# Kernel optimization log

Measured on AMD Instinct MI355X. Metric: run time of the kernel, lower is better.

The kernel has to match this reference:

```python
import jax, jax.numpy as jnp
import numpy as np

N_NODES = 50000
N_EDGES = 800000
IN_CH = 128
HID = 64
OUT_CH = 64


def sage_conv(x, src, dst, w_l, w_r, b, num_nodes):
    """PyG SAGEConv with mean aggregation: lin_l(mean_j x_j) + lin_r(x_i)."""
    # gather source features and scatter-mean into destination nodes
    agg = jax.ops.segment_sum(x[src], dst, num_segments=num_nodes)          # [N, C]
    deg = jax.ops.segment_sum(jnp.ones((src.shape[0],), x.dtype), dst,
                              num_segments=num_nodes)                        # [N]
    mean = agg / jnp.maximum(deg, 1.0)[:, None]
    return mean @ w_l + x @ w_r + b


def setup_inputs() -> dict:
    key = jax.random.key(0)
    k = jax.random.split(key, 8)
    x = jax.random.normal(k[0], (N_NODES, IN_CH), dtype=jnp.float32)
    edge_index = jax.random.randint(k[1], (2, N_EDGES), 0, N_NODES, dtype=jnp.int32)
    s1 = 1.0 / np.sqrt(IN_CH)
    s2 = 1.0 / np.sqrt(HID)
    w1_l = jax.random.uniform(k[2], (IN_CH, HID), jnp.float32, -s1, s1)
    w1_r = jax.random.uniform(k[3], (IN_CH, HID), jnp.float32, -s1, s1)
    b1 = jax.random.uniform(k[4], (HID,), jnp.float32, -s1, s1)
    w2_l = jax.random.uniform(k[5], (HID, OUT_CH), jnp.float32, -s2, s2)
    w2_r = jax.random.uniform(k[6], (HID, OUT_CH), jnp.float32, -s2, s2)
    b2 = jax.random.uniform(k[7], (OUT_CH,), jnp.float32, -s2, s2)
    return {"x": x, "edge_index": edge_index,
            "w1_l": w1_l, "w1_r": w1_r, "b1": b1,
            "w2_l": w2_l, "w2_r": w2_r, "b2": b2}


def reference(x, edge_index, w1_l, w1_r, b1, w2_l, w2_r, b2):
    src, dst = edge_index[0], edge_index[1]
    num_nodes = x.shape[0]
    h = jax.nn.relu(sage_conv(x, src, dst, w1_l, w1_r, b1, num_nodes))
    out = jax.nn.relu(sage_conv(h, src, dst, w2_l, w2_r, b2, num_nodes))
    return out
```

## Files before the change

### kernel.cpp

```cpp
#include <hip/hip_runtime.h>
#include <hip/hip_fp16.h>

#define DEGCAP 64
#define NB_MAX 256
#define BCAP 5120
#define TILE 4000

typedef _Float16 half8 __attribute__((ext_vector_type(8)));
typedef float float4v __attribute__((ext_vector_type(4)));

__global__ __launch_bounds__(256) void prep(int* __restrict__ bCursor,
                                            const float* __restrict__ w1l,
                                            const float* __restrict__ w1r,
                                            const float* __restrict__ w2l,
                                            const float* __restrict__ w2r,
                                            _Float16* __restrict__ Wt1,
                                            _Float16* __restrict__ Wt2) {
    const int gtid = blockIdx.x * 256 + threadIdx.x;
    const int gstride = gridDim.x * 256;
    if (gtid < NB_MAX) bCursor[gtid] = 0;
    for (int i = gtid; i < 128 * 128; i += gstride) {
        int c = i >> 7, k = i & 127;
        const float* W = (c < 64) ? w1l : w1r;
        Wt1[c * 128 + k] = (_Float16)W[k * 64 + (c & 63)];
    }
    for (int i = gtid; i < 128 * 64; i += gstride) {
        int c = i >> 6, k = i & 63;
        const float* W = (c < 64) ? w2l : w2r;
        Wt2[c * 64 + k] = (_Float16)W[k * 64 + (c & 63)];
    }
}

template <int K>
__device__ __forceinline__ void gemm_body_f32(const float* __restrict__ Av,
                                              const _Float16* __restrict__ Wt,
                                              unsigned short* __restrict__ Clh,
                                              unsigned short* __restrict__ Trh,
                                              int M, int blk) {
    constexpr int NS = K / 32;
    const int tid = threadIdx.x;
    const int row0 = blk * 64;
    const int wv = tid >> 6;
    const int lane = tid & 63;
    const int qd = lane >> 4;
    const int lr = lane & 15;
    const int col = wv * 16 + lr;

    half8 bl[NS], br[NS];
    #pragma unroll
    for (int s = 0; s < NS; ++s) {
        bl[s] = *(const half8*)&Wt[col * K + s * 32 + qd * 8];
        br[s] = *(const half8*)&Wt[(64 + col) * K + s * 32 + qd * 8];
    }

    half8 a[4][NS];
    #pragma unroll
    for (int i = 0; i < 4; ++i) {
        const int gr = row0 + i * 16 + lr;
        const bool ok = gr < M;
        const float* Arow = Av + (long long)gr * K;
        #pragma unroll
        for (int s = 0; s < NS; ++s) {
            float4 t0 = make_float4(0.f, 0.f, 0.f, 0.f);
            float4 t1 = make_float4(0.f, 0.f, 0.f, 0.f);
            if (ok) {
                t0 = *(const float4*)&Arow[s * 32 + qd * 8];
                t1 = *(const float4*)&Arow[s * 32 + qd * 8 + 4];
            }
            half8 h;
            h[0] = (_Float16)t0.x; h[1] = (_Float16)t0.y;
            h[2] = (_Float16)t0.z; h[3] = (_Float16)t0.w;
            h[4] = (_Float16)t1.x; h[5] = (_Float16)t1.y;
            h[6] = (_Float16)t1.z; h[7] = (_Float16)t1.w;
            a[i][s] = h;
        }
    }

    float4v accL[4], accR[4];
    #pragma unroll
    for (int i = 0; i < 4; ++i) {
        accL[i] = (float4v){0.f, 0.f, 0.f, 0.f};
        accR[i] = (float4v){0.f, 0.f, 0.f, 0.f};
    }

    #pragma unroll
    for (int i = 0; i < 4; ++i) {
        #pragma unroll
        for (int s = 0; s < NS; ++s) {
            accL[i] = __builtin_amdgcn_mfma_f32_16x16x32_f16(a[i][s], bl[s], accL[i], 0, 0, 0);
            accR[i] = __builtin_amdgcn_mfma_f32_16x16x32_f16(a[i][s], br[s], accR[i], 0, 0, 0);
        }
    }

    #pragma unroll
    for (int i = 0; i < 4; ++i) {
        #pragma unroll
        for (int rg = 0; rg < 4; ++rg) {
            int gr = row0 + i * 16 + qd * 4 + rg;
            if (gr < M) {
                Clh[(long long)gr * 64 + col] = __half_as_ushort(__float2half_rn(accL[i][rg]));
                Trh[(long long)gr * 64 + col] = __half_as_ushort(__float2half_rn(accR[i][rg]));
            }
        }
    }
}

__global__ __launch_bounds__(256) void fused_scatter_gemm1(
        const int* __restrict__ src, const int* __restrict__ dst,
        int* __restrict__ bCursor, unsigned int* __restrict__ gPacked,
        int E, int NB, int scatterBlocks,
        const float* __restrict__ A, const _Float16* __restrict__ Wt1,
        unsigned short* __restrict__ Clh, unsigned short* __restrict__ Trh,
        int M) {
    __shared__ __align__(16) char smem[22048];
    const int tid = threadIdx.x;

    if ((int)blockIdx.x < scatterBlocks) {
        unsigned int* spv = (unsigned int*)smem;
        unsigned char* sbuk = (unsigned char*)(smem + 16000);
        int* hist = (int*)(smem + 20000);
        int* cur  = (int*)(smem + 21024);

        const int t0 = blockIdx.x * TILE;
        const int len = (E - t0) < TILE ? (E - t0) : TILE;

        hist[tid] = 0;
        __syncthreads();
        for (int j = tid; j < len; j += 256) {
            int d = dst[t0 + j];
            int s = src[t0 + j];
            int b = d >> 8;
            sbuk[j] = (unsigned char)b;
            spv[j] = ((unsigned int)(d & 255) << 17) | (unsigned int)s;
            atomicAdd(&hist[b], 1);
        }
        __syncthreads();
        if (tid < NB && hist[tid] > 0)
            cur[tid] = tid * BCAP + atomicAdd(&bCursor[tid], hist[tid]);
        __syncthreads();
        for (int j = tid; j < len; j += 256) {
            int b = sbuk[j];
            int pos = atomicAdd(&cur[b], 1);
            if (pos < (b + 1) * BCAP) gPacked[pos] = spv[j];
        }
    } else {
        gemm_body_f32<128>(A, Wt1, Clh, Trh, M, (int)blockIdx.x - scatterBlocks);
    }
}

__global__ __launch_bounds__(256) void bucket_build(const unsigned int* __restrict__ gPacked,
                                                    const int* __restrict__ bCursor,
                                                    int* __restrict__ deg,
                                                    unsigned short* __restrict__ ssrc,
                                                    int N) {
    __shared__ int cnt[256];
    const int tid = threadIdx.x;
    const int b = blockIdx.x;
    const int base = b * BCAP;
    int C = bCursor[b];
    if (C > BCAP) C = BCAP;

    cnt[tid] = 0;
    __syncthreads();
    for (int j = tid; j < C; j += 256) {
        unsigned int v = gPacked[base + j];
        int ln = v >> 17;
        int pos = atomicAdd(&cnt[ln], 1);
        if (pos < DEGCAP)
            ssrc[(long long)(b * 256 + ln) * DEGCAP + pos] = (unsigned short)(v & 0x1FFFFu);
    }
    __syncthreads();
    int node = b * 256 + tid;
    if (node < N) deg[node] = cnt[tid] < DEGCAP ? cnt[tid] : DEGCAP;
}

__device__ __forceinline__ float4 agg_node(const uint2* __restrict__ TL,
                                           const uint2* __restrict__ TR,
                                           const float* __restrict__ bias,
                                           const int* __restrict__ deg_,
                                           const uint2* __restrict__ ssrc2,
                                           int w, int lane, int c, bool ok) {
    const int deg = ok ? deg_[w] : 0;
    const int n = deg < DEGCAP ? deg : DEGCAP;
    uint2 su = ok ? ssrc2[(size_t)w * 16 + c] : make_uint2(0u, 0u);

    float a0 = 0.f, a1 = 0.f, a2 = 0.f, a3 = 0.f;
    for (int j = 0; j < n; j += 4) {
        const int b = (lane & 48) + (j >> 2);
        unsigned sx = __shfl((int)su.x, b, 64);
        unsigned sy = __shfl((int)su.y, b, 64);
        int e0 = (int)(sx & 0xFFFFu);
        int e1 = (int)(sx >> 16);
        int e2 = (int)(sy & 0xFFFFu);
        int e3 = (int)(sy >> 16);
        uint2 q0 = TL[e0 * 16 + c];
        uint2 q1 = TL[e1 * 16 + c];
        uint2 q2 = TL[e2 * 16 + c];
        uint2 q3 = TL[e3 * 16 + c];
        float2 f;
        f = __half22float2(*(__half2*)&q0.x); a0 += f.x; a1 += f.y;
        f = __half22float2(*(__half2*)&q0.y); a2 += f.x; a3 += f.y;
        if (j + 1 < n) {
            f = __half22float2(*(__half2*)&q1.x); a0 += f.x; a1 += f.y;
            f = __half22float2(*(__half2*)&q1.y); a2 += f.x; a3 += f.y;
        }
        if (j + 2 < n) {
            f = __half22float2(*(__half2*)&q2.x); a0 += f.x; a1 += f.y;
            f = __half22float2(*(__half2*)&q2.y); a2 += f.x; a3 += f.y;
        }
        if (j + 3 < n) {
            f = __half22float2(*(__half2*)&q3.x); a0 += f.x; a1 += f.y;
            f = __half22float2(*(__half2*)&q3.y); a2 += f.x; a3 += f.y;
        }
    }

    float4 r = make_float4(0.f, 0.f, 0.f, 0.f);
    if (ok) {
        float d = (float)(deg > 1 ? deg : 1);
        uint2 tu = TR[(size_t)w * 16 + c];
        float2 t0 = __half22float2(*(__half2*)&tu.x);
        float2 t1 = __half22float2(*(__half2*)&tu.y);
        float4 bb = *(const float4*)&bias[c * 4];
        r.x = fmaxf(a0 / d + t0.x + bb.x, 0.f);
        r.y = fmaxf(a1 / d + t0.y + bb.y, 0.f);
        r.z = fmaxf(a2 / d + t1.x + bb.z, 0.f);
        r.w = fmaxf(a3 / d + t1.y + bb.w, 0.f);
    }
    return r;
}

__global__ __launch_bounds__(256) void agg1_gemm2(const uint2* __restrict__ TL,
                                                  const uint2* __restrict__ TR,
                                                  const float* __restrict__ b1,
                                                  const int* __restrict__ deg_,
                                                  const uint2* __restrict__ ssrc2,
                                                  const _Float16* __restrict__ Wt2,
                                                  unsigned short* __restrict__ Cl2,
                                                  unsigned short* __restrict__ Tr2,
                                                  int N) {
    __shared__ _Float16 xs[16 * 72];
    const int tid = threadIdx.x;
    const int wv = tid >> 6;
    const int lane = tid & 63;
    const int c = lane & 15;
    const int row = wv * 4 + (lane >> 4);
    const int w = (int)blockIdx.x * 16 + row;
    const bool ok = w < N;

    float4 h = agg_node(TL, TR, b1, deg_, ssrc2, w, lane, c, ok);
    {
        __half2 h0 = __floats2half2_rn(h.x, h.y);
        __half2 h1 = __floats2half2_rn(h.z, h.w);
        uint2 st;
        st.x = *(unsigned int*)&h0;
        st.y = *(unsigned int*)&h1;
        *(uint2*)&xs[row * 72 + c * 4] = st;
    }
    __syncthreads();

    const int qd = lane >> 4;
    const int lr = lane & 15;
    const int col = wv * 16 + lr;
    const int row0 = (int)blockIdx.x * 16;

    half8 bl[2], br[2], a[2];
    #pragma unroll
    for (int s = 0; s < 2; ++s) {
        bl[s] = *(const half8*)&Wt2[col * 64 + s * 32 + qd * 8];
        br[s] = *(const half8*)&Wt2[(64 + col) * 64 + s * 32 + qd * 8];
        a[s]  = *(const half8*)&xs[lr * 72 + s * 32 + qd * 8];
    }

    float4v accL = (float4v){0.f, 0.f, 0.f, 0.f};
    float4v accR = (float4v){0.f, 0.f, 0.f, 0.f};
    #pragma unroll
    for (int s = 0; s < 2; ++s) {
        accL = __builtin_amdgcn_mfma_f32_16x16x32_f16(a[s], bl[s], accL, 0, 0, 0);
        accR = __builtin_amdgcn_mfma_f32_16x16x32_f16(a[s], br[s], accR, 0, 0, 0);
    }

    #pragma unroll
    for (int rg = 0; rg < 4; ++rg) {
        int gr = row0 + qd * 4 + rg;
        if (gr < N) {
            Cl2[(long long)gr * 64 + col] = __half_as_ushort(__float2half_rn(accL[rg]));
            Tr2[(long long)gr * 64 + col] = __half_as_ushort(__float2half_rn(accR[rg]));
        }
    }
}

__global__ __launch_bounds__(256) void agg2(const uint2* __restrict__ TL,
                                            const uint2* __restrict__ TR,
                                            const float* __restrict__ bias,
                                            const int* __restrict__ deg_,
                                            const uint2* __restrict__ ssrc2,
                                            float* __restrict__ outv, int N) {
    const int tid = threadIdx.x;
    const int wv = tid >> 6;
    const int lane = tid & 63;
    const int c = lane & 15;
    const int w = (int)blockIdx.x * 16 + wv * 4 + (lane >> 4);
    const bool ok = w < N;

    float4 r = agg_node(TL, TR, bias, deg_, ssrc2, w, lane, c, ok);
    if (ok)
        ((float4*)outv)[(size_t)w * 16 + c] = r;
}

extern "C" void kernel_launch(void* const* d_in, const int* in_sizes, int n_in,
                              void* d_out, int out_size, void* d_ws, size_t ws_size,
                              hipStream_t stream) {
    const float* x   = (const float*)d_in[0];
    const int*   ei  = (const int*)d_in[1];
    const float* w1l = (const float*)d_in[2];
    const float* w1r = (const float*)d_in[3];
    const float* b1  = (const float*)d_in[4];
    const float* w2l = (const float*)d_in[5];
    const float* w2r = (const float*)d_in[6];
    const float* b2  = (const float*)d_in[7];
    float* out = (float*)d_out;

    const int N = in_sizes[0] / 128;
    const int E = in_sizes[1] / 2;
    const int* src = ei;
    const int* dst = ei + E;
    const int NB = (N + 255) >> 8;

    auto alignup = [](size_t v) { return (v + 255) & ~(size_t)255; };
    char* p = (char*)d_ws;
    int* bCursor = (int*)p;                    p += alignup(NB_MAX * sizeof(int));
    int* deg     = (int*)p;                    p += alignup((size_t)N * sizeof(int));
    unsigned int* gPacked = (unsigned int*)p;  p += alignup((size_t)NB_MAX * BCAP * sizeof(unsigned int));
    unsigned short* ssrc = (unsigned short*)p; p += alignup((size_t)N * DEGCAP * sizeof(unsigned short));
    const long long NC = (long long)N * 64;
    unsigned short* tlh = (unsigned short*)p;  p += alignup((size_t)NC * sizeof(unsigned short));
    unsigned short* tl2 = (unsigned short*)p;  p += alignup((size_t)NC * sizeof(unsigned short));
    unsigned short* trh = (unsigned short*)p;  p += alignup((size_t)NC * sizeof(unsigned short));
    unsigned short* tr2 = (unsigned short*)p;  p += alignup((size_t)NC * sizeof(unsigned short));
    _Float16* Wt1 = (_Float16*)p;              p += alignup(128 * 128 * sizeof(_Float16));
    _Float16* Wt2 = (_Float16*)p;              p += alignup(128 * 64 * sizeof(_Float16));

    const int scatterBlocks = (E + TILE - 1) / TILE;
    const int gemmBlocks = (N + 63) / 64;
    const int aggBlocks = (N + 15) / 16;

    prep<<<96, 256, 0, stream>>>(bCursor, w1l, w1r, w2l, w2r, Wt1, Wt2);

    fused_scatter_gemm1<<<scatterBlocks + gemmBlocks, 256, 0, stream>>>(
        src, dst, bCursor, gPacked, E, NB, scatterBlocks,
        x, Wt1, tlh, trh, N);

    bucket_build<<<NB, 256, 0, stream>>>(gPacked, bCursor, deg, ssrc, N);

    agg1_gemm2<<<aggBlocks, 256, 0, stream>>>((const uint2*)tlh,
                                              (const uint2*)trh,
                                              b1, deg, (const uint2*)ssrc,
                                              Wt2, tl2, tr2, N);

    agg2<<<aggBlocks, 256, 0, stream>>>((const uint2*)tl2,
                                        (const uint2*)tr2,
                                        b2, deg, (const uint2*)ssrc,
                                        out, N);
}
```

Before: 163.6 us.

## Fuse bucket build into layer-1 aggregation and second GEMM kernel

Merges the bucket_build kernel with agg1_gemm2: each block takes a 32-node slice of a 256-node bucket, builds that slice's neighbour lists in shared memory, writes them and the degrees out for agg2, then aggregates and runs the second-layer MFMA on 32 rows. This removes one kernel launch and the global round trip of the neighbour lists before layer 1. In exchange, each of the eight sub-blocks rescans the whole bucket's packed edge list and keeps only one eighth, so bucket reads rise eightfold. Grid parallelism also changes from N/16 blocks to NB*8 blocks of 32 nodes.

```diff
diff --git a/kernel.cpp b/kernel.cpp
--- a/kernel.cpp
+++ b/kernel.cpp
@@ -5,6 +5,7 @@
 #define NB_MAX 256
 #define BCAP 5120
 #define TILE 4000
+#define SUBB 8
 
 typedef _Float16 half8 __attribute__((ext_vector_type(8)));
 typedef float float4v __attribute__((ext_vector_type(4)));
@@ -148,30 +149,156 @@
     }
 }
 
-__global__ __launch_bounds__(256) void bucket_build(const unsigned int* __restrict__ gPacked,
-                                                    const int* __restrict__ bCursor,
-                                                    int* __restrict__ deg,
-                                                    unsigned short* __restrict__ ssrc,
-                                                    int N) {
-    __shared__ int cnt[256];
+__global__ __launch_bounds__(256) void bb_agg1_gemm2(
+        const unsigned int* __restrict__ gPacked,
+        const int* __restrict__ bCursor,
+        const uint2* __restrict__ TL, const uint2* __restrict__ TR,
+        const float* __restrict__ bias,
+        const _Float16* __restrict__ Wt2,
+        unsigned short* __restrict__ ssrc_out,
+        int* __restrict__ deg_out,
+        unsigned short* __restrict__ Cl2,
+        unsigned short* __restrict__ Tr2,
+        int N) {
+    __shared__ unsigned short ssrcT[32 * 64];
+    __shared__ int cnt[32];
+    __shared__ int degL[32];
+    __shared__ _Float16 xs[32 * 72];
     const int tid = threadIdx.x;
-    const int b = blockIdx.x;
-    const int base = b * BCAP;
-    int C = bCursor[b];
+    const int B = (int)blockIdx.x >> 3;
+    const int oct = (int)blockIdx.x & 7;
+    const int node0 = B * 256 + oct * 32;
+
+    if (tid < 32) cnt[tid] = 0;
+    __syncthreads();
+    int C = bCursor[B];
     if (C > BCAP) C = BCAP;
-
-    cnt[tid] = 0;
+    const unsigned int* gp = gPacked + B * BCAP;
+    for (int j = tid; j < C; j += 256) {
+        unsigned int v = gp[j];
+        int ln = v >> 17;
+        if ((ln >> 5) == oct) {
+            int l = ln & 31;
+            int pos = atomicAdd(&cnt[l], 1);
+            if (pos < DEGCAP)
+                ssrcT[l * 64 + pos] = (unsigned short)(v & 0x1FFFFu);
+        }
+    }
     __syncthreads();
-    for (int j = tid; j < C; j += 256) {
-        unsigned int v = gPacked[base + j];
-        int ln = v >> 17;
-        int pos = atomicAdd(&cnt[ln], 1);
-        if (pos < DEGCAP)
-            ssrc[(long long)(b * 256 + ln) * DEGCAP + pos] = (unsigned short)(v & 0x1FFFFu);
+    if (tid < 32) {
+        int d = cnt[tid] < DEGCAP ? cnt[tid] : DEGCAP;
+        degL[tid] = d;
+        int node = node0 + tid;
+        if (node < N) deg_out[node] = d;
     }
     __syncthreads();
-    int node = b * 256 + tid;
-    if (node < N) deg[node] = cnt[tid] < DEGCAP ? cnt[tid] : DEGCAP;
+    {
+        const uint2* s2 = (const uint2*)ssrcT;
+        for (int i = tid; i < 32 * 16; i += 256) {
+            int node = node0 + (i >> 4);
+            if (node < N)
+                ((uint2*)ssrc_out)[(size_t)node * 16 + (i & 15)] = s2[i];
+        }
+    }
+
+    const int wv = tid >> 6;
+    const int lane = tid & 63;
+    const int c = lane & 15;
+    const int g = lane >> 4;
+    for (int r = 0; r < 2; ++r) {
+        const int l = r * 16 + wv * 4 + g;
+        const int w = node0 + l;
+        const bool ok = w < N;
+        const int n = ok ? degL[l] : 0;
+        const unsigned short* row = &ssrcT[l * 64];
+        float a0 = 0.f, a1 = 0.f, a2 = 0.f, a3 = 0.f;
+        for (int j = 0; j < n; j += 4) {
+            uint2 ids = *(const uint2*)&row[j];
+            int e0 = (int)(ids.x & 0xFFFFu);
+            int e1 = (int)(ids.x >> 16);
+            int e2 = (int)(ids.y & 0xFFFFu);
+            int e3 = (int)(ids.y >> 16);
+            uint2 q0 = TL[e0 * 16 + c];
+            uint2 q1 = TL[e1 * 16 + c];
+            uint2 q2 = TL[e2 * 16 + c];
+            uint2 q3 = TL[e3 * 16 + c];
+            float2 f;
+            f = __half22float2(*(__half2*)&q0.x); a0 += f.x; a1 += f.y;
+            f = __half22float2(*(__half2*)&q0.y); a2 += f.x; a3 += f.y;
+            if (j + 1 < n) {
+                f = __half22float2(*(__half2*)&q1.x); a0 += f.x; a1 += f.y;
+                f = __half22float2(*(__half2*)&q1.y); a2 += f.x; a3 += f.y;
+            }
+            if (j + 2 < n) {
+                f = __half22float2(*(__half2*)&q2.x); a0 += f.x; a1 += f.y;
+                f = __half22float2(*(__half2*)&q2.y); a2 += f.x; a3 += f.y;
+            }
+            if (j + 3 < n) {
+                f = __half22float2(*(__half2*)&q3.x); a0 += f.x; a1 += f.y;
+                f = __half22float2(*(__half2*)&q3.y); a2 += f.x; a3 += f.y;
+            }
+        }
+        float4 h = make_float4(0.f, 0.f, 0.f, 0.f);
+        if (ok) {
+            float d = (float)(n > 1 ? n : 1);
+            uint2 tu = TR[(size_t)w * 16 + c];
+            float2 t0 = __half22float2(*(__half2*)&tu.x);
+            float2 t1 = __half22float2(*(__half2*)&tu.y);
+            float4 bb = *(const float4*)&bias[c * 4];
+            h.x = fmaxf(a0 / d + t0.x + bb.x, 0.f);
+            h.y = fmaxf(a1 / d + t0.y + bb.y, 0.f);
+            h.z = fmaxf(a2 / d + t1.x + bb.z, 0.f);
+            h.w = fmaxf(a3 / d + t1.y + bb.w, 0.f);
+        }
+        __half2 h0 = __floats2half2_rn(h.x, h.y);
+        __half2 h1 = __floats2half2_rn(h.z, h.w);
+        uint2 st;
+        st.x = *(unsigned int*)&h0;
+        st.y = *(unsigned int*)&h1;
+        *(uint2*)&xs[l * 72 + c * 4] = st;
+    }
+    __syncthreads();
+
+    const int qd = lane >> 4;
+    const int lr = lane & 15;
+    const int col = wv * 16 + lr;
+
+    half8 bl[2], br[2], a[2][2];
+    #pragma unroll
+    for (int s = 0; s < 2; ++s) {
+        bl[s] = *(const half8*)&Wt2[col * 64 + s * 32 + qd * 8];
+        br[s] = *(const half8*)&Wt2[(64 + col) * 64 + s * 32 + qd * 8];
+        #pragma unroll
+        for (int i = 0; i < 2; ++i)
+            a[i][s] = *(const half8*)&xs[(i * 16 + lr) * 72 + s * 32 + qd * 8];
+    }
+
+    float4v accL[2], accR[2];
+    #pragma unroll
+    for (int i = 0; i < 2; ++i) {
+        accL[i] = (float4v){0.f, 0.f, 0.f, 0.f};
+        accR[i] = (float4v){0.f, 0.f, 0.f, 0.f};
+    }
+    #pragma unroll
+    for (int i = 0; i < 2; ++i) {
+        #pragma unroll
+        for (int s = 0; s < 2; ++s) {
+            accL[i] = __builtin_amdgcn_mfma_f32_16x16x32_f16(a[i][s], bl[s], accL[i], 0, 0, 0);
+            accR[i] = __builtin_amdgcn_mfma_f32_16x16x32_f16(a[i][s], br[s], accR[i], 0, 0, 0);
+        }
+    }
+
+    #pragma unroll
+    for (int i = 0; i < 2; ++i) {
+        #pragma unroll
+        for (int rg = 0; rg < 4; ++rg) {
+            int gr = node0 + i * 16 + qd * 4 + rg;
+            if (gr < N) {
+                Cl2[(long long)gr * 64 + col] = __half_as_ushort(__float2half_rn(accL[i][rg]));
+                Tr2[(long long)gr * 64 + col] = __half_as_ushort(__float2half_rn(accR[i][rg]));
+            }
+        }
+    }
 }
 
 __device__ __forceinline__ float4 agg_node(const uint2* __restrict__ TL,
@@ -229,66 +356,6 @@
     return r;
 }
 
-__global__ __launch_bounds__(256) void agg1_gemm2(const uint2* __restrict__ TL,
-                                                  const uint2* __restrict__ TR,
-                                                  const float* __restrict__ b1,
-                                                  const int* __restrict__ deg_,
-                                                  const uint2* __restrict__ ssrc2,
-                                                  const _Float16* __restrict__ Wt2,
-                                                  unsigned short* __restrict__ Cl2,
-                                                  unsigned short* __restrict__ Tr2,
-                                                  int N) {
-    __shared__ _Float16 xs[16 * 72];
-    const int tid = threadIdx.x;
-    const int wv = tid >> 6;
-    const int lane = tid & 63;
-    const int c = lane & 15;
-    const int row = wv * 4 + (lane >> 4);
-    const int w = (int)blockIdx.x * 16 + row;
-    const bool ok = w < N;
-
-    float4 h = agg_node(TL, TR, b1, deg_, ssrc2, w, lane, c, ok);
-    {
-        __half2 h0 = __floats2half2_rn(h.x, h.y);
-        __half2 h1 = __floats2half2_rn(h.z, h.w);
-        uint2 st;
-        st.x = *(unsigned int*)&h0;
-        st.y = *(unsigned int*)&h1;
-        *(uint2*)&xs[row * 72 + c * 4] = st;
-    }
-    __syncthreads();
-
-    const int qd = lane >> 4;
-    const int lr = lane & 15;
-    const int col = wv * 16 + lr;
-    const int row0 = (int)blockIdx.x * 16;
-
-    half8 bl[2], br[2], a[2];
-    #pragma unroll
-    for (int s = 0; s < 2; ++s) {
-        bl[s] = *(const half8*)&Wt2[col * 64 + s * 32 + qd * 8];
-        br[s] = *(const half8*)&Wt2[(64 + col) * 64 + s * 32 + qd * 8];
-        a[s]  = *(const half8*)&xs[lr * 72 + s * 32 + qd * 8];
-    }
-
-    float4v accL = (float4v){0.f, 0.f, 0.f, 0.f};
-    float4v accR = (float4v){0.f, 0.f, 0.f, 0.f};
-    #pragma unroll
-    for (int s = 0; s < 2; ++s) {
-        accL = __builtin_amdgcn_mfma_f32_16x16x32_f16(a[s], bl[s], accL, 0, 0, 0);
-        accR = __builtin_amdgcn_mfma_f32_16x16x32_f16(a[s], br[s], accR, 0, 0, 0);
-    }
-
-    #pragma unroll
-    for (int rg = 0; rg < 4; ++rg) {
-        int gr = row0 + qd * 4 + rg;
-        if (gr < N) {
-            Cl2[(long long)gr * 64 + col] = __half_as_ushort(__float2half_rn(accL[rg]));
-            Tr2[(long long)gr * 64 + col] = __half_as_ushort(__float2half_rn(accR[rg]));
-        }
-    }
-}
-
 __global__ __launch_bounds__(256) void agg2(const uint2* __restrict__ TL,
                                             const uint2* __restrict__ TR,
                                             const float* __restrict__ bias,
@@ -343,6 +410,7 @@
     const int scatterBlocks = (E + TILE - 1) / TILE;
     const int gemmBlocks = (N + 63) / 64;
     const int aggBlocks = (N + 15) / 16;
+    const int bbaBlocks = NB * SUBB;
 
     prep<<<96, 256, 0, stream>>>(bCursor, w1l, w1r, w2l, w2r, Wt1, Wt2);
 
@@ -350,12 +418,9 @@
         src, dst, bCursor, gPacked, E, NB, scatterBlocks,
         x, Wt1, tlh, trh, N);
 
-    bucket_build<<<NB, 256, 0, stream>>>(gPacked, bCursor, deg, ssrc, N);
-
-    agg1_gemm2<<<aggBlocks, 256, 0, stream>>>((const uint2*)tlh,
-                                              (const uint2*)trh,
-                                              b1, deg, (const uint2*)ssrc,
-                                              Wt2, tl2, tr2, N);
+    bb_agg1_gemm2<<<bbaBlocks, 256, 0, stream>>>(
+        gPacked, bCursor, (const uint2*)tlh, (const uint2*)trh,
+        b1, Wt2, ssrc, deg, tl2, tr2, N);
 
     agg2<<<aggBlocks, 256, 0, stream>>>((const uint2*)tl2,
                                         (const uint2*)tr2,
```

Result: faster. 158.7 us (-3.0%).
